# Optimization experiments

Hardware: AMD Instinct MI355X
Metric: run time of the kernel (lower is better)

## Reference

```python
import jax, jax.numpy as jnp
import numpy as np

L = 3      # network layers, bpl = [1, B, B]
B = 2048   # buckets per layer (padded); layer 0 has 1 real bucket
S = 2048   # spigots per bucket; must equal next layer's bucket count
T = 16     # timesteps of precip forcing
G = 9.81


def setup_inputs() -> dict:
    key = jax.random.key(0)
    k1, k2, k3, k4 = jax.random.split(key, 4)
    u = jax.random.uniform(k1, (T,), jnp.float32)                  # precip per timestep
    theta = jax.random.uniform(k2, (L, B, S), jnp.float32)         # spigot coefficients
    # zero-pad theta exactly like initialize_theta_values: fake layer-0 buckets
    # (>0) and fake last-layer spigots (>0, last layer has 1 spigot) get theta=0
    bucket_mask = np.ones((L, B), np.float32); bucket_mask[0, 1:] = 0.0
    spigot_mask = np.ones((L, S), np.float32); spigot_mask[L - 1, 1:] = 0.0
    theta = theta * bucket_mask[:, :, None] * spigot_mask[:, None, :]
    spigots = jax.random.uniform(k3, (L, B, S, 2), jnp.float32)    # [..., (height, area)]
    H0 = jax.random.uniform(k4, (L, B), jnp.float32) + 1.0         # initial head per bucket
    return {"u": u, "theta": theta, "spigots": spigots, "H0": H0}


def _solve_layer(H, inflow, sp, th):
    """Vectorized solve_single_bucket over all B buckets of one layer.
    H, inflow: [B]; sp: [B,S,2]; th: [B,S]. Sequential recurrence over spigots."""
    Hb = H + inflow
    sp_h = jnp.transpose(sp[..., 0])   # [S,B]
    sp_a = jnp.transpose(sp[..., 1])   # [S,B]
    th_t = jnp.transpose(th)           # [S,B]

    def step(cum, xs):
        h_i, a_i, t_i = xs                       # each [B]
        H_eff = Hb - 0.5 * cum                   # H - sum(s_q[:i]) / 2
        h = jnp.maximum(0.0, H_eff - h_i)
        safe = jnp.where(h > 0, h, 1.0)          # grad-safe sqrt
        q = t_i * jnp.where(h > 0, jnp.sqrt(2.0 * G * safe), 0.0) * a_i
        return cum + q, q

    cum, qs = jax.lax.scan(step, jnp.zeros_like(Hb), (sp_h, sp_a, th_t))
    return Hb - cum, jnp.transpose(qs)           # new H [B], s_q [B,S]


def reference(u, theta, spigots, H0):
    def timestep(H, precip):
        ppl = precip / L                          # precip_inflow_per_layer
        s_q_prev = None
        Hs = []
        for l in range(L):
            if l == 0:
                # original: inflows = [precip_per_layer], single real bucket
                inflow = jnp.zeros((B,), H.dtype).at[0].set(ppl)
            else:
                # inflow[b] = sum_up s_q_prev[up, b] + ppl / n_buckets
                inflow = jnp.sum(s_q_prev, axis=0) + ppl / B
            Hn, s_q = _solve_layer(H[l], inflow, spigots[l], theta[l])
            Hs.append(Hn)
            s_q_prev = s_q
        outflow = jnp.sum(s_q_prev)               # network_outflow
        return jnp.stack(Hs), outflow

    _, outflows = jax.lax.scan(timestep, H0, u)
    return outflows                               # [T]
```

## Files before the change

### kernel.cpp

```cpp
#include <hip/hip_runtime.h>

#define NB 2048
#define NS 2048
#define NT 16
#define SQRT2G 4.4294469f
#define MHALF_SQRT2G -2.2147234f
#define PF 32

__device__ __forceinline__ float scan_bucket(const float2* P, int ps,
                                             float w, float* Q, int qs) {
    float2 A[PF], Bf[PF];
    const float2* Pp = P;
    float* Qp = Q;
    #pragma unroll
    for (int j = 0; j < PF; ++j) A[j] = Pp[(long)j * ps];
    Pp += (long)PF * ps;
    for (int sb = 0; sb < NS; sb += 2 * PF) {
        #pragma unroll
        for (int j = 0; j < PF; ++j) Bf[j] = Pp[(long)j * ps];
        Pp += (long)PF * ps;
        #pragma unroll
        for (int j = 0; j < PF; ++j) {
            float r = __builtin_amdgcn_sqrtf(fmaxf(w, 0.0f));
            Qp[(long)j * qs] = A[j].y * r;
            w = fmaf(A[j].y, r, w + A[j].x);
        }
        Qp += (long)PF * qs;
        if (sb + 2 * PF < NS) {
            #pragma unroll
            for (int j = 0; j < PF; ++j) A[j] = Pp[(long)j * ps];
            Pp += (long)PF * ps;
        }
        #pragma unroll
        for (int j = 0; j < PF; ++j) {
            float r = __builtin_amdgcn_sqrtf(fmaxf(w, 0.0f));
            Qp[(long)j * qs] = Bf[j].y * r;
            w = fmaf(Bf[j].y, r, w + Bf[j].x);
        }
        Qp += (long)PF * qs;
    }
    return w;
}

__global__ __launch_bounds__(256, 1) void prep_kernel(
        const float* __restrict__ u,
        const float* __restrict__ theta, const float2* __restrict__ sp,
        const float* __restrict__ H0,
        float2* __restrict__ P1, float2* __restrict__ PL0, float2* __restrict__ P2,
        float* __restrict__ H1, float* __restrict__ H2,
        float* __restrict__ h01, float* __restrict__ H00, float* __restrict__ h00f,
        float* __restrict__ Q0) {
    int blk = blockIdx.x, tid = threadIdx.x;
    if (blk < 1024) {
        __shared__ float2 tile[64][65];
        int bt = blk >> 5, st = blk & 31;
        int ls = tid & 63, rb = tid >> 6;
        #pragma unroll 4
        for (int r = 0; r < 16; ++r) {
            int bl = rb + 4 * r;
            int b = bt * 64 + bl, s = st * 64 + ls;
            long idx = (long)(NB + b) * NS + s;
            float2 v = sp[idx];
            float hn = (s == NS - 1) ? 0.0f : sp[idx + 1].x;
            float mc = theta[idx] * v.y * MHALF_SQRT2G;
            tile[bl][ls] = make_float2(v.x - hn, mc);
            if (s == 0) h01[b] = v.x;
        }
        __syncthreads();
        int lb = tid & 63, rs = tid >> 6;
        #pragma unroll 4
        for (int r = 0; r < 16; ++r) {
            int sl = rs + 4 * r;
            int s = st * 64 + sl, b = bt * 64 + lb;
            P1[(long)s * NB + b] = tile[lb][sl];
        }
    } else if (blk < 1032) {
        int s = (blk - 1024) * 256 + tid;
        float2 v = sp[s];
        float hn = (s == NS - 1) ? 0.0f : sp[s + 1].x;
        PL0[s] = make_float2(v.x - hn, theta[s] * v.y * MHALF_SQRT2G);
        if (s == 0) *h00f = v.x;
    } else if (blk < 1040) {
        int b = (blk - 1032) * 256 + tid;
        long idx = (long)(2 * NB + b) * NS;
        float2 v = sp[idx];
        P2[b] = make_float2(v.x, theta[idx] * v.y * SQRT2G);
    } else if (blk < 1056) {
        int i = (blk - 1040) * 256 + tid;
        if (i < NB) H1[i] = H0[NB + i];
        else        H2[i - NB] = H0[2 * NB + (i - NB)];
    } else {
        __shared__ float2 L0[NS];
        for (int j = tid; j < NS; j += 256) {
            float2 v = sp[j];
            float hn = (j == NS - 1) ? 0.0f : sp[j + 1].x;
            L0[j] = make_float2(v.x - hn, theta[j] * v.y * MHALF_SQRT2G);
        }
        __syncthreads();
        if (tid == 0) {
            float Hb = H0[0] + u[0] * (1.0f / 3.0f);
            float w = scan_bucket(L0, 1, Hb - sp[0].x, Q0, 1);
            *H00 = 2.0f * w - Hb;
        }
    }
}

__global__ __launch_bounds__(64, 1) void step_kernel(
        int k, const float* __restrict__ u,
        const float2* __restrict__ P1, const float2* __restrict__ PL0,
        const float2* __restrict__ P2,
        float* __restrict__ Qa, float* __restrict__ Qb, float* __restrict__ Q0,
        float* __restrict__ H1, float* __restrict__ H2,
        const float* __restrict__ h01, float* __restrict__ H00,
        const float* __restrict__ h00f,
        float* __restrict__ out) {
    int blk = blockIdx.x, tid = threadIdx.x;
    if (blk < 32) {
        if (k >= NT) return;
        int b = blk * 64 + tid;
        float* Qw = (k & 1) ? Qb : Qa;
        float inflow = fmaf(-2.0f, Q0[k * NB + b], u[k] * (1.0f / (3.0f * (float)NB)));
        float Hb = H1[b] + inflow;
        float w = scan_bucket(P1 + b, NB, Hb - h01[b], Qw + b, NB);
        H1[b] = 2.0f * w - Hb;
    } else if (blk == 32) {
        if (k + 1 >= NT) return;
        if (tid == 0) {
            float Hb = *H00 + u[k + 1] * (1.0f / 3.0f);
            float w = scan_bucket(PL0, 1, Hb - *h00f, Q0 + (k + 1) * NB, 1);
            *H00 = 2.0f * w - Hb;
        }
    } else {
        int t = k - 1;
        if (t < 0) return;
        const float* Qr = (t & 1) ? Qb : Qa;
        int r = blk - 33;
        float ppl_B = u[t] * (1.0f / (3.0f * (float)NB));
        float qacc = 0.0f;
        for (int i = 0; i < 16; ++i) {
            int b = r * 16 + i;
            const float* row = Qr + (long)b * NB;
            float s0 = 0.f, s1 = 0.f, s2 = 0.f, s3 = 0.f;
            for (int j = 0; j < NB; j += 256) {
                s0 += row[j + tid];
                s1 += row[j + 64 + tid];
                s2 += row[j + 128 + tid];
                s3 += row[j + 192 + tid];
            }
            float s = (s0 + s1) + (s2 + s3);
            #pragma unroll
            for (int m = 32; m >= 1; m >>= 1) s += __shfl_xor(s, m, 64);
            if (tid == 0) {
                float Hb = H2[b] + fmaf(-2.0f, s, ppl_B);
                float h = fmaxf(Hb - P2[b].x, 0.0f);
                float q = P2[b].y * __builtin_amdgcn_sqrtf(h);
                H2[b] = Hb - q;
                qacc += q;
            }
        }
        if (tid == 0) atomicAdd(out + t, qacc);
    }
}

extern "C" void kernel_launch(void* const* d_in, const int* in_sizes, int n_in,
                              void* d_out, int out_size, void* d_ws, size_t ws_size,
                              hipStream_t stream) {
    const float*  u     = (const float*)d_in[0];
    const float*  theta = (const float*)d_in[1];
    const float2* sp    = (const float2*)d_in[2];
    const float*  H0    = (const float*)d_in[3];
    float* out = (float*)d_out;

    float* ws   = (float*)d_ws;
    float2* P1  = (float2*)ws;
    float*  Qa  = ws + (size_t)2 * NS * NB;
    float*  Qb  = Qa + (size_t)NS * NB;
    float2* PL0 = (float2*)(Qb + (size_t)NS * NB);
    float2* P2  = PL0 + NS;
    float*  Q0  = (float*)(P2 + NB);
    float*  H1  = Q0 + (size_t)NT * NB;
    float*  H2  = H1 + NB;
    float*  h01 = H2 + NB;
    float*  H00 = h01 + NB;
    float*  h00f= H00 + 1;

    hipMemsetAsync(d_out, 0, (size_t)out_size * sizeof(float), stream);

    prep_kernel<<<1057, 256, 0, stream>>>(u, theta, sp, H0, P1, PL0, P2,
                                          H1, H2, h01, H00, h00f, Q0);
    for (int k = 0; k <= NT; ++k) {
        step_kernel<<<161, 64, 0, stream>>>(k, u, P1, PL0, P2, Qa, Qb, Q0,
                                            H1, H2, h01, H00, h00f, out);
    }
}
```

Baseline: 1.283 ms.

## Pack spigot pairs into float4 and stream layer scans through LDS

Spigot parameters are repacked so each 16-byte element holds two consecutive spigots. The layer-1 bucket scan now double-buffers 16-row chunks into LDS with global_load_lds and manual vmcnt waits, overlapping loads with the serial sqrt recurrence. Outflows are written as float4 quads, and the layer-2 reduction processes four downstream buckets per row, cutting reduction blocks from 128 to 32. The gain depends on hand-placed waitcnt correctness and on LDS reads not stalling the serial dependency chain.

```diff
diff --git a/kernel.cpp b/kernel.cpp
--- a/kernel.cpp
+++ b/kernel.cpp
@@ -5,39 +5,60 @@
 #define NT 16
 #define SQRT2G 4.4294469f
 #define MHALF_SQRT2G -2.2147234f
-#define PF 32
-
-__device__ __forceinline__ float scan_bucket(const float2* P, int ps,
-                                             float w, float* Q, int qs) {
-    float2 A[PF], Bf[PF];
+
+typedef float f4 __attribute__((ext_vector_type(4)));
+
+__device__ __forceinline__ void gll16(const f4* g, f4* l) {
+    __builtin_amdgcn_global_load_lds(
+        (const __attribute__((address_space(1))) unsigned int*)g,
+        (__attribute__((address_space(3))) unsigned int*)l, 16, 0, 0);
+}
+
+#define QUAD(p0, p1, QS)                                          \
+    {                                                             \
+        float r0 = __builtin_amdgcn_sqrtf(fmaxf(w, 0.0f));        \
+        float q0 = p0.y * r0; w = fmaf(p0.y, r0, w + p0.x);       \
+        float r1 = __builtin_amdgcn_sqrtf(fmaxf(w, 0.0f));        \
+        float q1 = p0.w * r1; w = fmaf(p0.w, r1, w + p0.z);       \
+        float r2 = __builtin_amdgcn_sqrtf(fmaxf(w, 0.0f));        \
+        float q2 = p1.y * r2; w = fmaf(p1.y, r2, w + p1.x);       \
+        float r3 = __builtin_amdgcn_sqrtf(fmaxf(w, 0.0f));        \
+        float q3 = p1.w * r3; w = fmaf(p1.w, r3, w + p1.z);       \
+        f4 qv; qv.x = q0; qv.y = q1; qv.z = q2; qv.w = q3;        \
+        qp[(size_t)jj * (QS)] = qv;                               \
+    }
+
+#define SPF 32
+__device__ __forceinline__ float scan_simple(const float2* P, float w, float* Q) {
+    float2 A[SPF], Bf[SPF];
     const float2* Pp = P;
     float* Qp = Q;
     #pragma unroll
-    for (int j = 0; j < PF; ++j) A[j] = Pp[(long)j * ps];
-    Pp += (long)PF * ps;
-    for (int sb = 0; sb < NS; sb += 2 * PF) {
-        #pragma unroll
-        for (int j = 0; j < PF; ++j) Bf[j] = Pp[(long)j * ps];
-        Pp += (long)PF * ps;
-        #pragma unroll
-        for (int j = 0; j < PF; ++j) {
+    for (int j = 0; j < SPF; ++j) A[j] = Pp[j];
+    Pp += SPF;
+    for (int sb = 0; sb < NS; sb += 2 * SPF) {
+        #pragma unroll
+        for (int j = 0; j < SPF; ++j) Bf[j] = Pp[j];
+        Pp += SPF;
+        #pragma unroll
+        for (int j = 0; j < SPF; ++j) {
             float r = __builtin_amdgcn_sqrtf(fmaxf(w, 0.0f));
-            Qp[(long)j * qs] = A[j].y * r;
+            Qp[j] = A[j].y * r;
             w = fmaf(A[j].y, r, w + A[j].x);
         }
-        Qp += (long)PF * qs;
-        if (sb + 2 * PF < NS) {
-            #pragma unroll
-            for (int j = 0; j < PF; ++j) A[j] = Pp[(long)j * ps];
-            Pp += (long)PF * ps;
-        }
-        #pragma unroll
-        for (int j = 0; j < PF; ++j) {
+        Qp += SPF;
+        if (sb + 2 * SPF < NS) {
+            #pragma unroll
+            for (int j = 0; j < SPF; ++j) A[j] = Pp[j];
+            Pp += SPF;
+        }
+        #pragma unroll
+        for (int j = 0; j < SPF; ++j) {
             float r = __builtin_amdgcn_sqrtf(fmaxf(w, 0.0f));
-            Qp[(long)j * qs] = Bf[j].y * r;
+            Qp[j] = Bf[j].y * r;
             w = fmaf(Bf[j].y, r, w + Bf[j].x);
         }
-        Qp += (long)PF * qs;
+        Qp += SPF;
     }
     return w;
 }
@@ -46,7 +67,7 @@
         const float* __restrict__ u,
         const float* __restrict__ theta, const float2* __restrict__ sp,
         const float* __restrict__ H0,
-        float2* __restrict__ P1, float2* __restrict__ PL0, float2* __restrict__ P2,
+        f4* __restrict__ P1q, f4* __restrict__ PL0q, float2* __restrict__ P2,
         float* __restrict__ H1, float* __restrict__ H2,
         float* __restrict__ h01, float* __restrict__ H00, float* __restrict__ h00f,
         float* __restrict__ Q0) {
@@ -69,37 +90,42 @@
         __syncthreads();
         int lb = tid & 63, rs = tid >> 6;
         #pragma unroll 4
-        for (int r = 0; r < 16; ++r) {
-            int sl = rs + 4 * r;
-            int s = st * 64 + sl, b = bt * 64 + lb;
-            P1[(long)s * NB + b] = tile[lb][sl];
-        }
-    } else if (blk < 1032) {
-        int s = (blk - 1024) * 256 + tid;
-        float2 v = sp[s];
-        float hn = (s == NS - 1) ? 0.0f : sp[s + 1].x;
-        PL0[s] = make_float2(v.x - hn, theta[s] * v.y * MHALF_SQRT2G);
-        if (s == 0) *h00f = v.x;
-    } else if (blk < 1040) {
-        int b = (blk - 1032) * 256 + tid;
+        for (int r = 0; r < 8; ++r) {
+            int sq = rs + 4 * r;
+            float2 e0 = tile[lb][2 * sq], e1 = tile[lb][2 * sq + 1];
+            f4 val; val.x = e0.x; val.y = e0.y; val.z = e1.x; val.w = e1.y;
+            P1q[(size_t)(st * 32 + sq) * NB + bt * 64 + lb] = val;
+        }
+    } else if (blk < 1028) {
+        int pi = (blk - 1024) * 256 + tid;
+        int s0 = 2 * pi;
+        float2 v0 = sp[s0], v1 = sp[s0 + 1];
+        float h2 = (s0 + 2 < NS) ? sp[s0 + 2].x : 0.0f;
+        f4 val;
+        val.x = v0.x - v1.x; val.y = theta[s0] * v0.y * MHALF_SQRT2G;
+        val.z = v1.x - h2;   val.w = theta[s0 + 1] * v1.y * MHALF_SQRT2G;
+        PL0q[pi] = val;
+        if (pi == 0) *h00f = v0.x;
+    } else if (blk < 1036) {
+        int b = (blk - 1028) * 256 + tid;
         long idx = (long)(2 * NB + b) * NS;
         float2 v = sp[idx];
         P2[b] = make_float2(v.x, theta[idx] * v.y * SQRT2G);
-    } else if (blk < 1056) {
-        int i = (blk - 1040) * 256 + tid;
+    } else if (blk < 1052) {
+        int i = (blk - 1036) * 256 + tid;
         if (i < NB) H1[i] = H0[NB + i];
         else        H2[i - NB] = H0[2 * NB + (i - NB)];
     } else {
-        __shared__ float2 L0[NS];
+        __shared__ float2 L0buf[NS];
         for (int j = tid; j < NS; j += 256) {
             float2 v = sp[j];
             float hn = (j == NS - 1) ? 0.0f : sp[j + 1].x;
-            L0[j] = make_float2(v.x - hn, theta[j] * v.y * MHALF_SQRT2G);
+            L0buf[j] = make_float2(v.x - hn, theta[j] * v.y * MHALF_SQRT2G);
         }
         __syncthreads();
         if (tid == 0) {
             float Hb = H0[0] + u[0] * (1.0f / 3.0f);
-            float w = scan_bucket(L0, 1, Hb - sp[0].x, Q0, 1);
+            float w = scan_simple((const float2*)L0buf, Hb - sp[0].x, Q0);
             *H00 = 2.0f * w - Hb;
         }
     }
@@ -107,58 +133,134 @@
 
 __global__ __launch_bounds__(64, 1) void step_kernel(
         int k, const float* __restrict__ u,
-        const float2* __restrict__ P1, const float2* __restrict__ PL0,
+        const f4* __restrict__ P1q, const f4* __restrict__ PL0q,
         const float2* __restrict__ P2,
-        float* __restrict__ Qa, float* __restrict__ Qb, float* __restrict__ Q0,
+        f4* __restrict__ Qa, f4* __restrict__ Qb, float* __restrict__ Q0,
         float* __restrict__ H1, float* __restrict__ H2,
         const float* __restrict__ h01, float* __restrict__ H00,
         const float* __restrict__ h00f,
         float* __restrict__ out) {
-    int blk = blockIdx.x, tid = threadIdx.x;
+    __shared__ f4 SA[16 * 64];
+    __shared__ f4 SB[16 * 64];
+    int blk = blockIdx.x, lane = threadIdx.x;
     if (blk < 32) {
         if (k >= NT) return;
-        int b = blk * 64 + tid;
-        float* Qw = (k & 1) ? Qb : Qa;
+        int b = blk * 64 + lane;
+        f4* Qw = (k & 1) ? Qb : Qa;
         float inflow = fmaf(-2.0f, Q0[k * NB + b], u[k] * (1.0f / (3.0f * (float)NB)));
         float Hb = H1[b] + inflow;
-        float w = scan_bucket(P1 + b, NB, Hb - h01[b], Qw + b, NB);
+        float w = Hb - h01[b];
+        const f4* gp = P1q + b;
+        #pragma unroll
+        for (int j = 0; j < 16; ++j) gll16(gp + (size_t)j * NB, SA + j * 64);
+        gp += (size_t)16 * NB;
+        #pragma unroll
+        for (int j = 0; j < 16; ++j) gll16(gp + (size_t)j * NB, SB + j * 64);
+        gp += (size_t)16 * NB;
+        f4* qp = Qw + b;
+        for (int ip = 0; ip < 31; ++ip) {
+            asm volatile("s_waitcnt vmcnt(16)" ::: "memory");
+            __builtin_amdgcn_sched_barrier(0);
+            #pragma unroll
+            for (int jj = 0; jj < 8; ++jj) {
+                f4 p0 = SA[(2 * jj) * 64 + lane], p1 = SA[(2 * jj + 1) * 64 + lane];
+                QUAD(p0, p1, NB)
+            }
+            qp += (size_t)8 * NB;
+            #pragma unroll
+            for (int j = 0; j < 16; ++j) gll16(gp + (size_t)j * NB, SA + j * 64);
+            gp += (size_t)16 * NB;
+            asm volatile("s_waitcnt vmcnt(16)" ::: "memory");
+            __builtin_amdgcn_sched_barrier(0);
+            #pragma unroll
+            for (int jj = 0; jj < 8; ++jj) {
+                f4 p0 = SB[(2 * jj) * 64 + lane], p1 = SB[(2 * jj + 1) * 64 + lane];
+                QUAD(p0, p1, NB)
+            }
+            qp += (size_t)8 * NB;
+            #pragma unroll
+            for (int j = 0; j < 16; ++j) gll16(gp + (size_t)j * NB, SB + j * 64);
+            gp += (size_t)16 * NB;
+        }
+        asm volatile("s_waitcnt vmcnt(16)" ::: "memory");
+        __builtin_amdgcn_sched_barrier(0);
+        #pragma unroll
+        for (int jj = 0; jj < 8; ++jj) {
+            f4 p0 = SA[(2 * jj) * 64 + lane], p1 = SA[(2 * jj + 1) * 64 + lane];
+            QUAD(p0, p1, NB)
+        }
+        qp += (size_t)8 * NB;
+        asm volatile("s_waitcnt vmcnt(0)" ::: "memory");
+        __builtin_amdgcn_sched_barrier(0);
+        #pragma unroll
+        for (int jj = 0; jj < 8; ++jj) {
+            f4 p0 = SB[(2 * jj) * 64 + lane], p1 = SB[(2 * jj + 1) * 64 + lane];
+            QUAD(p0, p1, NB)
+        }
         H1[b] = 2.0f * w - Hb;
     } else if (blk == 32) {
         if (k + 1 >= NT) return;
-        if (tid == 0) {
+        #pragma unroll
+        for (int j = 0; j < 16; ++j) gll16(PL0q + j * 64 + lane, SA + j * 64);
+        asm volatile("s_waitcnt vmcnt(0)" ::: "memory");
+        __builtin_amdgcn_sched_barrier(0);
+        if (lane == 0) {
             float Hb = *H00 + u[k + 1] * (1.0f / 3.0f);
-            float w = scan_bucket(PL0, 1, Hb - *h00f, Q0 + (k + 1) * NB, 1);
+            float w = Hb - *h00f;
+            f4* qp = (f4*)(Q0 + (size_t)(k + 1) * NB);
+            for (int bi = 0; bi < 64; ++bi) {
+                f4 P[16];
+                #pragma unroll
+                for (int j = 0; j < 16; ++j) P[j] = SA[bi * 16 + j];
+                #pragma unroll
+                for (int jj = 0; jj < 8; ++jj) {
+                    f4 p0 = P[2 * jj], p1 = P[2 * jj + 1];
+                    QUAD(p0, p1, 1)
+                }
+                qp += 8;
+            }
             *H00 = 2.0f * w - Hb;
         }
     } else {
         int t = k - 1;
         if (t < 0) return;
-        const float* Qr = (t & 1) ? Qb : Qa;
+        const f4* Qr = (t & 1) ? Qb : Qa;
         int r = blk - 33;
         float ppl_B = u[t] * (1.0f / (3.0f * (float)NB));
         float qacc = 0.0f;
-        for (int i = 0; i < 16; ++i) {
-            int b = r * 16 + i;
-            const float* row = Qr + (long)b * NB;
-            float s0 = 0.f, s1 = 0.f, s2 = 0.f, s3 = 0.f;
-            for (int j = 0; j < NB; j += 256) {
-                s0 += row[j + tid];
-                s1 += row[j + 64 + tid];
-                s2 += row[j + 128 + tid];
-                s3 += row[j + 192 + tid];
-            }
-            float s = (s0 + s1) + (s2 + s3);
-            #pragma unroll
-            for (int m = 32; m >= 1; m >>= 1) s += __shfl_xor(s, m, 64);
-            if (tid == 0) {
-                float Hb = H2[b] + fmaf(-2.0f, s, ppl_B);
-                float h = fmaxf(Hb - P2[b].x, 0.0f);
-                float q = P2[b].y * __builtin_amdgcn_sqrtf(h);
-                H2[b] = Hb - q;
-                qacc += q;
-            }
-        }
-        if (tid == 0) atomicAdd(out + t, qacc);
+        for (int ql = 0; ql < 16; ++ql) {
+            int qr = r * 16 + ql;
+            const f4* row = Qr + (size_t)qr * NB;
+            f4 a0 = {0,0,0,0}, a1 = {0,0,0,0}, a2 = {0,0,0,0}, a3 = {0,0,0,0};
+            #pragma unroll
+            for (int kk = 0; kk < 32; kk += 4) {
+                a0 += row[lane + 64 * kk];
+                a1 += row[lane + 64 * (kk + 1)];
+                a2 += row[lane + 64 * (kk + 2)];
+                a3 += row[lane + 64 * (kk + 3)];
+            }
+            f4 acc = (a0 + a1) + (a2 + a3);
+            #pragma unroll
+            for (int m = 32; m >= 1; m >>= 1) {
+                acc.x += __shfl_xor(acc.x, m, 64);
+                acc.y += __shfl_xor(acc.y, m, 64);
+                acc.z += __shfl_xor(acc.z, m, 64);
+                acc.w += __shfl_xor(acc.w, m, 64);
+            }
+            if (lane == 0) {
+                float infl[4] = {acc.x, acc.y, acc.z, acc.w};
+                #pragma unroll
+                for (int c = 0; c < 4; ++c) {
+                    int b2 = qr * 4 + c;
+                    float Hb = H2[b2] + fmaf(-2.0f, infl[c], ppl_B);
+                    float h = fmaxf(Hb - P2[b2].x, 0.0f);
+                    float q = P2[b2].y * __builtin_amdgcn_sqrtf(h);
+                    H2[b2] = Hb - q;
+                    qacc += q;
+                }
+            }
+        }
+        if (lane == 0) atomicAdd(out + t, qacc);
     }
 }
 
@@ -172,24 +274,25 @@
     float* out = (float*)d_out;
 
     float* ws   = (float*)d_ws;
-    float2* P1  = (float2*)ws;
-    float*  Qa  = ws + (size_t)2 * NS * NB;
-    float*  Qb  = Qa + (size_t)NS * NB;
-    float2* PL0 = (float2*)(Qb + (size_t)NS * NB);
-    float2* P2  = PL0 + NS;
-    float*  Q0  = (float*)(P2 + NB);
-    float*  H1  = Q0 + (size_t)NT * NB;
-    float*  H2  = H1 + NB;
-    float*  h01 = H2 + NB;
-    float*  H00 = h01 + NB;
-    float*  h00f= H00 + 1;
+    f4*    P1q  = (f4*)ws;
+    float* Qa_f = ws + (size_t)2 * NS * NB;
+    float* Qb_f = Qa_f + (size_t)NS * NB;
+    f4*    PL0q = (f4*)(Qb_f + (size_t)NS * NB);
+    float2* P2  = (float2*)(PL0q + NS / 2);
+    float* Q0   = (float*)(P2 + NB);
+    float* H1   = Q0 + (size_t)NT * NB;
+    float* H2   = H1 + NB;
+    float* h01  = H2 + NB;
+    float* H00  = h01 + NB;
+    float* h00f = H00 + 1;
 
     hipMemsetAsync(d_out, 0, (size_t)out_size * sizeof(float), stream);
 
-    prep_kernel<<<1057, 256, 0, stream>>>(u, theta, sp, H0, P1, PL0, P2,
+    prep_kernel<<<1053, 256, 0, stream>>>(u, theta, sp, H0, P1q, PL0q, P2,
                                           H1, H2, h01, H00, h00f, Q0);
     for (int k = 0; k <= NT; ++k) {
-        step_kernel<<<161, 64, 0, stream>>>(k, u, P1, PL0, P2, Qa, Qb, Q0,
-                                            H1, H2, h01, H00, h00f, out);
-    }
-}
+        step_kernel<<<65, 64, 0, stream>>>(k, u, P1q, PL0q, P2,
+                                           (f4*)Qa_f, (f4*)Qb_f, Q0,
+                                           H1, H2, h01, H00, h00f, out);
+    }
+}
```

Result: faster. 1.059 ms (-17.4%).
